# Optimization experiments

Measured on AMD Instinct MI355X. Metric: run time of the kernel, lower is better.

## Reference

```python
import jax, jax.numpy as jnp
import numpy as np

B, T, V = 32, 100, 20000
E, H, M, DD = 128, 128, 64, 2


def setup_inputs() -> dict:
    key = jax.random.key(0)
    ks = jax.random.split(key, 12)
    x = jax.random.uniform(ks[0], (B, T, V), dtype=jnp.float32)
    # zero out trailing timesteps per example so Masking layer matters
    lens = jax.random.randint(ks[1], (B,), T * 3 // 4, T + 1)
    tmask = (jnp.arange(T)[None, :] < lens[:, None]).astype(jnp.float32)
    x = x * tmask[:, :, None]
    a = jax.random.uniform(ks[2], (B, V), dtype=jnp.float32)
    d = jax.random.normal(ks[3], (B, DD), dtype=jnp.float32)
    # parameters
    emb = jax.random.uniform(ks[4], (V, E), minval=-0.1, maxval=0.1, dtype=jnp.float32)
    s = 1.0 / np.sqrt(E)
    gru_k = jax.random.uniform(ks[5], (E, 3 * H), minval=-s, maxval=s, dtype=jnp.float32)
    gru_rk = jax.random.normal(ks[6], (H, 3 * H), dtype=jnp.float32) / np.sqrt(H)
    gru_b_i = jnp.zeros((3 * H,), jnp.float32)   # input bias (reset_after=True)
    gru_b_r = jnp.zeros((3 * H,), jnp.float32)   # recurrent bias
    s1 = 1.0 / np.sqrt(H + E)
    W1 = jax.random.uniform(ks[7], (H + E, M), minval=-s1, maxval=s1, dtype=jnp.float32)
    b1 = jnp.zeros((M,), jnp.float32)
    s2 = 1.0 / np.sqrt(M + DD)
    W2 = jax.random.uniform(ks[8], (M + DD, 1), minval=-s2, maxval=s2, dtype=jnp.float32)
    b2 = jnp.zeros((1,), jnp.float32)
    return dict(x=x, a=a, d=d, emb=emb, gru_k=gru_k, gru_rk=gru_rk,
                gru_b_i=gru_b_i, gru_b_r=gru_b_r, W1=W1, b1=b1, W2=W2, b2=b2)


def _gru_final_state(xe, mask, gru_k, gru_rk, gru_b_i, gru_b_r):
    # xe: [B,T,E], mask: [B,T] bool. Keras GRU, reset_after=True, eval mode (dropout off).
    Hn = gru_rk.shape[0]
    x_proj = jnp.einsum('bte,eh->bth', xe, gru_k) + gru_b_i  # [B,T,3H]

    def step(h, inp):
        xp_t, m_t = inp                      # [B,3H], [B]
        rec = h @ gru_rk + gru_b_r           # [B,3H]
        xz, xr, xh = jnp.split(xp_t, 3, axis=-1)
        rz, rr, rh = jnp.split(rec, 3, axis=-1)
        z = jax.nn.sigmoid(xz + rz)
        r = jax.nn.sigmoid(xr + rr)
        hh = jnp.tanh(xh + r * rh)
        h_new = z * h + (1.0 - z) * hh
        h = jnp.where(m_t[:, None], h_new, h)  # masked steps carry state
        return h, None

    h0 = jnp.zeros((xe.shape[0], Hn), xe.dtype)
    h_final, _ = jax.lax.scan(step, h0, (jnp.swapaxes(x_proj, 0, 1), jnp.swapaxes(mask, 0, 1)))
    return h_final


def reference(x, a, d, emb, gru_k, gru_rk, gru_b_i, gru_b_r, W1, b1, W2, b2):
    ae = jnp.tanh(a @ emb)                       # [B,E]
    xe = jnp.tanh(jnp.einsum('btv,ve->bte', x, emb))  # [B,T,E]
    mask = jnp.any(xe != 0.0, axis=-1)           # Masking(mask_value=0.0)
    h = _gru_final_state(xe, mask, gru_k, gru_rk, gru_b_i, gru_b_r)  # [B,H]
    c = jnp.tanh(jnp.concatenate([h, ae], axis=1) @ W1 + b1)         # [B,M]
    out = jax.nn.sigmoid(jnp.concatenate([c, d], axis=1) @ W2 + b2)  # [B,1]
    return out
```

## Files before the change

kernel.cpp:

```cpp
#include <hip/hip_runtime.h>

typedef __attribute__((ext_vector_type(8))) short short8;
typedef __attribute__((ext_vector_type(4))) float float4v;

#define V_ 20000
#define KS 32

__device__ __forceinline__ unsigned short f2bf(float f) {
    union { float f; unsigned int u; } v; v.f = f;
    unsigned int u = v.u;
    u += 0x7fffu + ((u >> 16) & 1u);
    return (unsigned short)(u >> 16);
}

__device__ __forceinline__ float fast_tanh(float x) {
    float xc = fminf(15.f, fmaxf(-15.f, x));
    float e = __expf(2.f * xc);
    return (e - 1.f) / (e + 1.f);
}

__device__ __forceinline__ float sigmoidf_(float x) {
    float xc = fminf(30.f, fmaxf(-30.f, x));
    return 1.f / (1.f + __expf(-xc));
}

__global__ __launch_bounds__(256) void cvt_embT(const float* __restrict__ emb,
                                                unsigned short* __restrict__ embT) {
    __shared__ unsigned short tile[128 * 65];
    int tid = threadIdx.x;
    int k0 = blockIdx.x * 64;
    const float4v* e4 = (const float4v*)emb;
    #pragma unroll
    for (int c = 0; c < 8; ++c) {
        int l4 = c * 256 + tid;
        int k = l4 >> 5;
        int n4 = l4 & 31;
        float4v f = {0.f, 0.f, 0.f, 0.f};
        if (k0 + k < V_) f = e4[(size_t)(k0 + k) * 32 + n4];
        tile[(n4 * 4 + 0) * 65 + k] = f2bf(f.x);
        tile[(n4 * 4 + 1) * 65 + k] = f2bf(f.y);
        tile[(n4 * 4 + 2) * 65 + k] = f2bf(f.z);
        tile[(n4 * 4 + 3) * 65 + k] = f2bf(f.w);
    }
    __syncthreads();
    #pragma unroll
    for (int c = 0; c < 4; ++c) {
        int l8 = c * 256 + tid;
        int n = l8 >> 3, seg = l8 & 7;
        int kk = k0 + seg * 8;
        if (kk < V_) {
            short8 v;
            #pragma unroll
            for (int i = 0; i < 8; ++i) v[i] = (short)tile[n * 65 + seg * 8 + i];
            *(short8*)(embT + (size_t)n * V_ + kk) = v;
        }
    }
}

__global__ __launch_bounds__(256, 3) void big_gemm(const float* __restrict__ x,
                                                   const float* __restrict__ a,
                                                   const unsigned short* __restrict__ embT,
                                                   float* __restrict__ partial) {
    int tid = threadIdx.x;
    int w = tid >> 6, lane = tid & 63;
    int ln = lane & 15, quad = lane >> 4;
    int tile = blockIdx.x * 4 + w;
    if (tile > 100) return;
    int by = blockIdx.y;
    int r0 = tile * 32;

    int kb0 = by * 19 + (by < 17 ? by : 17);
    int cnt = 19 + (by < 17 ? 1 : 0);

    const float* __restrict__ src0;
    const float* __restrict__ src1;
    if (r0 < 3200) {
        src0 = x + (size_t)(r0 + ln) * V_;
        src1 = x + (size_t)(r0 + 16 + ln) * V_;
    } else {
        src0 = a + (size_t)ln * V_;
        src1 = a + (size_t)(16 + ln) * V_;
    }
    const unsigned short* __restrict__ bp0 = embT + (size_t)ln * V_ + quad * 8;

    float4v acc[2][8];
    #pragma unroll
    for (int f = 0; f < 2; ++f)
        #pragma unroll
        for (int t = 0; t < 8; ++t) acc[f][t] = (float4v){0.f, 0.f, 0.f, 0.f};

    int kq = kb0 * 32 + quad * 8;
    float4v a00 = *(const float4v*)(src0 + kq);
    float4v a01 = *(const float4v*)(src0 + kq + 4);
    float4v a10 = *(const float4v*)(src1 + kq);
    float4v a11 = *(const float4v*)(src1 + kq + 4);

    for (int s = 0; s < cnt; ++s) {
        int k = (kb0 + s) * 32;
        float4v n00, n01, n10, n11;
        if (s + 1 < cnt) {
            int knq = k + 32 + quad * 8;
            n00 = *(const float4v*)(src0 + knq);
            n01 = *(const float4v*)(src0 + knq + 4);
            n10 = *(const float4v*)(src1 + knq);
            n11 = *(const float4v*)(src1 + knq + 4);
        }
        short8 bf[8];
        #pragma unroll
        for (int t = 0; t < 8; ++t)
            bf[t] = *(const short8*)(bp0 + (size_t)t * 16 * V_ + k);
        short8 pa0, pa1;
        pa0[0]=(short)f2bf(a00.x); pa0[1]=(short)f2bf(a00.y); pa0[2]=(short)f2bf(a00.z); pa0[3]=(short)f2bf(a00.w);
        pa0[4]=(short)f2bf(a01.x); pa0[5]=(short)f2bf(a01.y); pa0[6]=(short)f2bf(a01.z); pa0[7]=(short)f2bf(a01.w);
        pa1[0]=(short)f2bf(a10.x); pa1[1]=(short)f2bf(a10.y); pa1[2]=(short)f2bf(a10.z); pa1[3]=(short)f2bf(a10.w);
        pa1[4]=(short)f2bf(a11.x); pa1[5]=(short)f2bf(a11.y); pa1[6]=(short)f2bf(a11.z); pa1[7]=(short)f2bf(a11.w);
        #pragma unroll
        for (int t = 0; t < 8; ++t) {
            acc[0][t] = __builtin_amdgcn_mfma_f32_16x16x32_bf16(pa0, bf[t], acc[0][t], 0, 0, 0);
            acc[1][t] = __builtin_amdgcn_mfma_f32_16x16x32_bf16(pa1, bf[t], acc[1][t], 0, 0, 0);
        }
        a00 = n00; a01 = n01; a10 = n10; a11 = n11;
    }

    float* dst = partial + ((size_t)by * 3232 + r0 + quad * 4) * 128 + ln;
    #pragma unroll
    for (int f = 0; f < 2; ++f) {
        #pragma unroll
        for (int t = 0; t < 8; ++t) {
            #pragma unroll
            for (int reg = 0; reg < 4; ++reg)
                dst[(size_t)(f * 16 + reg) * 128 + t * 16] = acc[f][t][reg];
        }
    }
}

__global__ __launch_bounds__(128) void reduce_tanh(const float* __restrict__ partial,
                                                   float* __restrict__ xe,
                                                   float* __restrict__ ae,
                                                   float* __restrict__ maskg) {
    int row = blockIdx.x;
    int e = threadIdx.x;
    float s = 0.f;
    #pragma unroll
    for (int k = 0; k < KS; ++k)
        s += partial[((size_t)k * 3232 + row) * 128 + e];
    float v = fast_tanh(s);
    if (row < 3200) {
        xe[(size_t)row * 128 + e] = v;
        __shared__ int any;
        if (e == 0) any = 0;
        __syncthreads();
        if (v != 0.f) any = 1;
        __syncthreads();
        if (e == 0) maskg[row] = any ? 1.f : 0.f;
    } else {
        ae[(row - 3200) * 128 + e] = v;
    }
}

__global__ __launch_bounds__(384) void xproj_kernel(const float* __restrict__ xe,
                                                    const float* __restrict__ gru_k,
                                                    const float* __restrict__ b_i,
                                                    float* __restrict__ xproj) {
    __shared__ float xs[16 * 128];
    int tid = threadIdx.x;
    int row0 = blockIdx.x * 16;
    const float4v* src = (const float4v*)(xe + (size_t)row0 * 128);
    float4v* dstl = (float4v*)xs;
    #pragma unroll
    for (int c = 0; c < 2; ++c) {
        int i4 = c * 384 + tid;
        if (i4 < 512) dstl[i4] = src[i4];
    }
    __syncthreads();
    int j = tid;
    float acc[16];
    #pragma unroll
    for (int r = 0; r < 16; ++r) acc[r] = 0.f;
    float bi = b_i[j];
    for (int k4 = 0; k4 < 32; ++k4) {
        float g0 = gru_k[(k4 * 4 + 0) * 384 + j];
        float g1 = gru_k[(k4 * 4 + 1) * 384 + j];
        float g2 = gru_k[(k4 * 4 + 2) * 384 + j];
        float g3 = gru_k[(k4 * 4 + 3) * 384 + j];
        #pragma unroll
        for (int r = 0; r < 16; ++r) {
            float4v xv = *(const float4v*)&xs[r * 128 + k4 * 4];
            acc[r] = fmaf(xv.x, g0, acc[r]);
            acc[r] = fmaf(xv.y, g1, acc[r]);
            acc[r] = fmaf(xv.z, g2, acc[r]);
            acc[r] = fmaf(xv.w, g3, acc[r]);
        }
    }
    #pragma unroll
    for (int r = 0; r < 16; ++r)
        xproj[(size_t)(row0 + r) * 384 + j] = acc[r] + bi;
}

__global__ __launch_bounds__(384) void gru_kernel(const float* __restrict__ xproj,
                                                  const float* __restrict__ maskg,
                                                  const float* __restrict__ gru_rk,
                                                  const float* __restrict__ b_r,
                                                  float* __restrict__ hout) {
    int b = blockIdx.x;
    int j = threadIdx.x;
    float w[128];
    #pragma unroll
    for (int k = 0; k < 128; ++k) w[k] = gru_rk[k * 384 + j];
    float br = b_r[j];
    __shared__ float4v hs4[32];
    __shared__ float recs[384];
    float* hs = (float*)hs4;
    float hreg = 0.f;
    if (j < 128) hs[j] = 0.f;
    const float* xp_base = xproj + (size_t)b * 100 * 384;
    const float* mk = maskg + b * 100;
    float xz = 0.f, xr = 0.f, xh = 0.f;
    if (j < 128) { xz = xp_base[j]; xr = xp_base[128 + j]; xh = xp_base[256 + j]; }
    __syncthreads();
    for (int t = 0; t < 100; ++t) {
        float nxz = 0.f, nxr = 0.f, nxh = 0.f;
        if (t < 99 && j < 128) {
            const float* nb = xp_base + (t + 1) * 384;
            nxz = nb[j]; nxr = nb[128 + j]; nxh = nb[256 + j];
        }
        float s0 = 0.f, s1 = 0.f, s2 = 0.f, s3 = 0.f;
        #pragma unroll
        for (int k4 = 0; k4 < 32; ++k4) {
            float4v hv = hs4[k4];
            s0 = fmaf(hv.x, w[k4 * 4 + 0], s0);
            s1 = fmaf(hv.y, w[k4 * 4 + 1], s1);
            s2 = fmaf(hv.z, w[k4 * 4 + 2], s2);
            s3 = fmaf(hv.w, w[k4 * 4 + 3], s3);
        }
        recs[j] = br + ((s0 + s1) + (s2 + s3));
        __syncthreads();
        if (j < 128) {
            float z = sigmoidf_(xz + recs[j]);
            float r = sigmoidf_(xr + recs[128 + j]);
            float hh = fast_tanh(xh + r * recs[256 + j]);
            float hn = z * hreg + (1.f - z) * hh;
            hreg = (mk[t] != 0.f) ? hn : hreg;
            hs[j] = hreg;
        }
        __syncthreads();
        xz = nxz; xr = nxr; xh = nxh;
    }
    if (j < 128) hout[b * 128 + j] = hreg;
}

__global__ __launch_bounds__(64) void head_kernel(const float* __restrict__ hout,
                                                  const float* __restrict__ ae,
                                                  const float* __restrict__ d,
                                                  const float* __restrict__ W1,
                                                  const float* __restrict__ b1,
                                                  const float* __restrict__ W2,
                                                  const float* __restrict__ b2,
                                                  float* __restrict__ out) {
    int b = blockIdx.x;
    int m = threadIdx.x;
    float s = b1[m];
    const float* hb = hout + b * 128;
    const float* ab = ae + b * 128;
    #pragma unroll 4
    for (int k = 0; k < 128; ++k) s = fmaf(hb[k], W1[k * 64 + m], s);
    #pragma unroll 4
    for (int k = 0; k < 128; ++k) s = fmaf(ab[k], W1[(128 + k) * 64 + m], s);
    float c = fast_tanh(s);
    float p = c * W2[m];
    #pragma unroll
    for (int off = 32; off > 0; off >>= 1) p += __shfl_down(p, off);
    if (m == 0) {
        p += d[b * 2 + 0] * W2[64] + d[b * 2 + 1] * W2[65] + b2[0];
        out[b] = sigmoidf_(p);
    }
}

extern "C" void kernel_launch(void* const* d_in, const int* in_sizes, int n_in,
                              void* d_out, int out_size, void* d_ws, size_t ws_size,
                              hipStream_t stream) {
    (void)in_sizes; (void)n_in; (void)out_size; (void)ws_size;
    const float* x      = (const float*)d_in[0];
    const float* a      = (const float*)d_in[1];
    const float* d      = (const float*)d_in[2];
    const float* emb    = (const float*)d_in[3];
    const float* gru_k  = (const float*)d_in[4];
    const float* gru_rk = (const float*)d_in[5];
    const float* gbi    = (const float*)d_in[6];
    const float* gbr    = (const float*)d_in[7];
    const float* W1     = (const float*)d_in[8];
    const float* b1     = (const float*)d_in[9];
    const float* W2     = (const float*)d_in[10];
    const float* b2     = (const float*)d_in[11];
    float* out = (float*)d_out;

    char* ws = (char*)d_ws;
    unsigned short* embT = (unsigned short*)(ws);
    float* xe      = (float*)(ws + 5120000);
    float* ae      = (float*)(ws + 6758400);
    float* maskg   = (float*)(ws + 6774784);
    float* xproj   = (float*)(ws + 6787584);
    float* hout    = (float*)(ws + 11702784);
    float* partial = (float*)(ws + 11719168);

    hipLaunchKernelGGL(cvt_embT,    dim3(313),      dim3(256), 0, stream, emb, embT);
    hipLaunchKernelGGL(big_gemm,    dim3(26, KS),   dim3(256), 0, stream, x, a, embT, partial);
    hipLaunchKernelGGL(reduce_tanh, dim3(3232),     dim3(128), 0, stream, partial, xe, ae, maskg);
    hipLaunchKernelGGL(xproj_kernel,dim3(200),      dim3(384), 0, stream, xe, gru_k, gbi, xproj);
    hipLaunchKernelGGL(gru_kernel,  dim3(32),       dim3(384), 0, stream, xproj, maskg, gru_rk, gbr, hout);
    hipLaunchKernelGGL(head_kernel, dim3(32),       dim3(64),  0, stream, hout, ae, d, W1, b1, W2, b2, out);
}
```

Before: 605.9 us.

## Restructure big GEMM with LDS double-buffered A tiles and fewer K-splits

Rewrites the embedding GEMM so each block handles 16 rows and all 128 output columns. The fp32 activation rows are converted to bf16 once into a double-buffered LDS tile, and all four waves share it for their MFMAs. The K-split count drops from 32 to 8, which cuts the partial-sum buffer written by the GEMM and read back by the reduction. In exchange, each wave holds fewer accumulators, the embedding matrix is re-read by more blocks, and the unguarded B loads past each split's K range rely on the zero-filled A lanes.

```diff
diff --git a/kernel.cpp b/kernel.cpp
--- a/kernel.cpp
+++ b/kernel.cpp
@@ -4,7 +4,9 @@
 typedef __attribute__((ext_vector_type(4))) float float4v;
 
 #define V_ 20000
-#define KS 32
+#define KS 8
+#define NT 10
+#define LSTR 264
 
 __device__ __forceinline__ unsigned short f2bf(float f) {
     union { float f; unsigned int u; } v; v.f = f;
@@ -57,80 +59,103 @@
     }
 }
 
-__global__ __launch_bounds__(256, 3) void big_gemm(const float* __restrict__ x,
-                                                   const float* __restrict__ a,
-                                                   const unsigned short* __restrict__ embT,
-                                                   float* __restrict__ partial) {
+__global__ __launch_bounds__(256) void big_gemm(const float* __restrict__ x,
+                                                const float* __restrict__ a,
+                                                const unsigned short* __restrict__ embT,
+                                                float* __restrict__ partial) {
+    __shared__ unsigned short Alds[2][16 * LSTR];
     int tid = threadIdx.x;
     int w = tid >> 6, lane = tid & 63;
     int ln = lane & 15, quad = lane >> 4;
-    int tile = blockIdx.x * 4 + w;
-    if (tile > 100) return;
-    int by = blockIdx.y;
-    int r0 = tile * 32;
-
-    int kb0 = by * 19 + (by < 17 ? by : 17);
-    int cnt = 19 + (by < 17 ? 1 : 0);
-
-    const float* __restrict__ src0;
-    const float* __restrict__ src1;
-    if (r0 < 3200) {
-        src0 = x + (size_t)(r0 + ln) * V_;
-        src1 = x + (size_t)(r0 + 16 + ln) * V_;
-    } else {
-        src0 = a + (size_t)ln * V_;
-        src1 = a + (size_t)(16 + ln) * V_;
-    }
-    const unsigned short* __restrict__ bp0 = embT + (size_t)ln * V_ + quad * 8;
-
-    float4v acc[2][8];
-    #pragma unroll
-    for (int f = 0; f < 2; ++f)
+    int bx = blockIdx.x, by = blockIdx.y;
+    int r0 = bx * 16;
+
+    int ustart = by * 78 + (by < 1 ? by : 1);
+    int nu = 78 + (by < 1 ? 1 : 0);
+    int kbase = ustart * 32;
+    int klen = nu * 32;
+
+    const float* srcP[4];
+    #pragma unroll
+    for (int j = 0; j < 4; ++j) {
+        int rg = r0 + w + 4 * j;
+        const float* base = (rg < 3200) ? (x + (size_t)rg * V_)
+                                        : (a + (size_t)(rg - 3200) * V_);
+        srcP[j] = base + kbase + lane * 4;
+    }
+    const unsigned short* bp0 = embT + (size_t)((w * 2 + 0) * 16 + ln) * V_ + kbase + quad * 8;
+    const unsigned short* bp1 = embT + (size_t)((w * 2 + 1) * 16 + ln) * V_ + kbase + quad * 8;
+
+    float4v acc0 = {0.f, 0.f, 0.f, 0.f};
+    float4v acc1 = {0.f, 0.f, 0.f, 0.f};
+    float4v f0, f1, f2, f3;
+
+    int wbr = w + 0;
+
+    f0 = *(const float4v*)(srcP[0]);
+    f1 = *(const float4v*)(srcP[1]);
+    f2 = *(const float4v*)(srcP[2]);
+    f3 = *(const float4v*)(srcP[3]);
+    {
+        unsigned short* dst = &Alds[0][lane * 4];
+        unsigned short s[16];
+        s[0]=f2bf(f0.x); s[1]=f2bf(f0.y); s[2]=f2bf(f0.z); s[3]=f2bf(f0.w);
+        s[4]=f2bf(f1.x); s[5]=f2bf(f1.y); s[6]=f2bf(f1.z); s[7]=f2bf(f1.w);
+        s[8]=f2bf(f2.x); s[9]=f2bf(f2.y); s[10]=f2bf(f2.z); s[11]=f2bf(f2.w);
+        s[12]=f2bf(f3.x); s[13]=f2bf(f3.y); s[14]=f2bf(f3.z); s[15]=f2bf(f3.w);
         #pragma unroll
-        for (int t = 0; t < 8; ++t) acc[f][t] = (float4v){0.f, 0.f, 0.f, 0.f};
-
-    int kq = kb0 * 32 + quad * 8;
-    float4v a00 = *(const float4v*)(src0 + kq);
-    float4v a01 = *(const float4v*)(src0 + kq + 4);
-    float4v a10 = *(const float4v*)(src1 + kq);
-    float4v a11 = *(const float4v*)(src1 + kq + 4);
-
-    for (int s = 0; s < cnt; ++s) {
-        int k = (kb0 + s) * 32;
-        float4v n00, n01, n10, n11;
-        if (s + 1 < cnt) {
-            int knq = k + 32 + quad * 8;
-            n00 = *(const float4v*)(src0 + knq);
-            n01 = *(const float4v*)(src0 + knq + 4);
-            n10 = *(const float4v*)(src1 + knq);
-            n11 = *(const float4v*)(src1 + knq + 4);
-        }
-        short8 bf[8];
+        for (int j = 0; j < 4; ++j) {
+            int rr = wbr + 4 * j;
+            *(uint2*)&dst[rr * LSTR] = *(uint2*)&s[j * 4];
+        }
+    }
+    __syncthreads();
+
+    for (int t = 0; t < NT; ++t) {
+        int buf = t & 1;
+        bool more = (t + 1 < NT);
+        if (more) {
+            int nlim = klen - (t + 1) * 256;
+            bool ok = (lane * 4 < nlim);
+            int off = (t + 1) * 256;
+            float4v z = {0.f, 0.f, 0.f, 0.f};
+            f0 = ok ? *(const float4v*)(srcP[0] + off) : z;
+            f1 = ok ? *(const float4v*)(srcP[1] + off) : z;
+            f2 = ok ? *(const float4v*)(srcP[2] + off) : z;
+            f3 = ok ? *(const float4v*)(srcP[3] + off) : z;
+        }
+        const unsigned short* al = &Alds[buf][ln * LSTR + quad * 8];
+        const unsigned short* b0p = bp0 + t * 256;
+        const unsigned short* b1p = bp1 + t * 256;
         #pragma unroll
-        for (int t = 0; t < 8; ++t)
-            bf[t] = *(const short8*)(bp0 + (size_t)t * 16 * V_ + k);
-        short8 pa0, pa1;
-        pa0[0]=(short)f2bf(a00.x); pa0[1]=(short)f2bf(a00.y); pa0[2]=(short)f2bf(a00.z); pa0[3]=(short)f2bf(a00.w);
-        pa0[4]=(short)f2bf(a01.x); pa0[5]=(short)f2bf(a01.y); pa0[6]=(short)f2bf(a01.z); pa0[7]=(short)f2bf(a01.w);
-        pa1[0]=(short)f2bf(a10.x); pa1[1]=(short)f2bf(a10.y); pa1[2]=(short)f2bf(a10.z); pa1[3]=(short)f2bf(a10.w);
-        pa1[4]=(short)f2bf(a11.x); pa1[5]=(short)f2bf(a11.y); pa1[6]=(short)f2bf(a11.z); pa1[7]=(short)f2bf(a11.w);
-        #pragma unroll
-        for (int t = 0; t < 8; ++t) {
-            acc[0][t] = __builtin_amdgcn_mfma_f32_16x16x32_bf16(pa0, bf[t], acc[0][t], 0, 0, 0);
-            acc[1][t] = __builtin_amdgcn_mfma_f32_16x16x32_bf16(pa1, bf[t], acc[1][t], 0, 0, 0);
-        }
-        a00 = n00; a01 = n01; a10 = n10; a11 = n11;
+        for (int kk = 0; kk < 8; ++kk) {
+            short8 af = *(const short8*)(al + kk * 32);
+            short8 bf0 = *(const short8*)(b0p + kk * 32);
+            short8 bf1 = *(const short8*)(b1p + kk * 32);
+            acc0 = __builtin_amdgcn_mfma_f32_16x16x32_bf16(af, bf0, acc0, 0, 0, 0);
+            acc1 = __builtin_amdgcn_mfma_f32_16x16x32_bf16(af, bf1, acc1, 0, 0, 0);
+        }
+        if (more) {
+            unsigned short* dst = &Alds[buf ^ 1][lane * 4];
+            unsigned short s[16];
+            s[0]=f2bf(f0.x); s[1]=f2bf(f0.y); s[2]=f2bf(f0.z); s[3]=f2bf(f0.w);
+            s[4]=f2bf(f1.x); s[5]=f2bf(f1.y); s[6]=f2bf(f1.z); s[7]=f2bf(f1.w);
+            s[8]=f2bf(f2.x); s[9]=f2bf(f2.y); s[10]=f2bf(f2.z); s[11]=f2bf(f2.w);
+            s[12]=f2bf(f3.x); s[13]=f2bf(f3.y); s[14]=f2bf(f3.z); s[15]=f2bf(f3.w);
+            #pragma unroll
+            for (int j = 0; j < 4; ++j) {
+                int rr = wbr + 4 * j;
+                *(uint2*)&dst[rr * LSTR] = *(uint2*)&s[j * 4];
+            }
+        }
+        __syncthreads();
     }
 
     float* dst = partial + ((size_t)by * 3232 + r0 + quad * 4) * 128 + ln;
     #pragma unroll
-    for (int f = 0; f < 2; ++f) {
-        #pragma unroll
-        for (int t = 0; t < 8; ++t) {
-            #pragma unroll
-            for (int reg = 0; reg < 4; ++reg)
-                dst[(size_t)(f * 16 + reg) * 128 + t * 16] = acc[f][t][reg];
-        }
+    for (int reg = 0; reg < 4; ++reg) {
+        dst[(size_t)reg * 128 + (w * 2 + 0) * 16] = acc0[reg];
+        dst[(size_t)reg * 128 + (w * 2 + 1) * 16] = acc1[reg];
     }
 }
 
@@ -304,7 +329,7 @@
     float* partial = (float*)(ws + 11719168);
 
     hipLaunchKernelGGL(cvt_embT,    dim3(313),      dim3(256), 0, stream, emb, embT);
-    hipLaunchKernelGGL(big_gemm,    dim3(26, KS),   dim3(256), 0, stream, x, a, embT, partial);
+    hipLaunchKernelGGL(big_gemm,    dim3(202, KS),  dim3(256), 0, stream, x, a, embT, partial);
     hipLaunchKernelGGL(reduce_tanh, dim3(3232),     dim3(128), 0, stream, partial, xe, ae, maskg);
     hipLaunchKernelGGL(xproj_kernel,dim3(200),      dim3(384), 0, stream, xe, gru_k, gbi, xproj);
     hipLaunchKernelGGL(gru_kernel,  dim3(32),       dim3(384), 0, stream, xproj, maskg, gru_rk, gbr, hout);
```

New measurement: 597.4 us. About the same (-1.4%).
